# Optimization experiments

Hardware: AMD Instinct MI355X
Metric: run time of the kernel (lower is better)

## Reference

```python
import jax, jax.numpy as jnp
import numpy as np

H = 256       # hidden_dim
DICT = 30     # dict_size
SOS = 1       # symb2int['<sos>']

def gru_cell(x, h, Wih, Whh, bih, bhh):
    # PyTorch GRU cell math
    gi = x @ Wih.T + bih
    gh = h @ Whh.T + bhh
    ir, iz, inn = jnp.split(gi, 3, axis=-1)
    hr, hz, hn = jnp.split(gh, 3, axis=-1)
    r = jax.nn.sigmoid(ir + hr)
    z = jax.nn.sigmoid(iz + hz)
    n = jnp.tanh(inn + r * hn)
    return (1.0 - z) * n + z * h

def run_gru(xs, h0, Wih, Whh, bih, bhh):
    # xs: [T, B, F] -> outputs [T, B, Hc], final hidden [B, Hc]
    def step(h, x):
        h = gru_cell(x, h, Wih, Whh, bih, bhh)
        return h, h
    hT, out = jax.lax.scan(step, h0, xs)
    return out, hT

def setup_inputs() -> dict:
    key = jax.random.key(0)
    ks = jax.random.split(key, 24)
    B, T, L = 128, 512, 64
    se = 1.0 / np.sqrt(H)        # encoder GRU init scale
    sd = 1.0 / np.sqrt(2 * H)    # decoder GRU / linears scale
    def r(k, shape, sc):
        return jax.random.normal(k, shape, jnp.float32) * sc
    return {
        "x": jax.random.normal(ks[0], (B, T, 2), jnp.float32),
        "target_seq": jax.random.randint(ks[1], (B, L), 0, DICT),
        # encoder GRU, forward direction
        "enc_Wih_f": r(ks[2], (3 * H, 2), se), "enc_Whh_f": r(ks[3], (3 * H, H), se),
        "enc_bih_f": r(ks[4], (3 * H,), se),   "enc_bhh_f": r(ks[5], (3 * H,), se),
        # encoder GRU, backward direction
        "enc_Wih_b": r(ks[6], (3 * H, 2), se), "enc_Whh_b": r(ks[7], (3 * H, H), se),
        "enc_bih_b": r(ks[8], (3 * H,), se),   "enc_bhh_b": r(ks[9], (3 * H,), se),
        # decoder embedding + GRU (hidden 2H)
        "emb": r(ks[10], (DICT, H), 1.0),
        "dec_Wih": r(ks[11], (6 * H, H), sd),     "dec_Whh": r(ks[12], (6 * H, 2 * H), sd),
        "dec_bih": r(ks[13], (6 * H,), sd),       "dec_bhh": r(ks[14], (6 * H,), sd),
        # hidden2query, att_combine, fc
        "Wq": r(ks[15], (2 * H, 2 * H), sd), "bq": r(ks[16], (2 * H,), sd),
        "Wc": r(ks[17], (H, 4 * H), sd),     "bc": r(ks[18], (H,), sd),
        "Wf": r(ks[19], (DICT, H), se),      "bf": r(ks[20], (DICT,), se),
    }

def reference(x, target_seq,
              enc_Wih_f, enc_Whh_f, enc_bih_f, enc_bhh_f,
              enc_Wih_b, enc_Whh_b, enc_bih_b, enc_bhh_b,
              emb, dec_Wih, dec_Whh, dec_bih, dec_bhh,
              Wq, bq, Wc, bc, Wf, bf):
    B = x.shape[0]
    xs = jnp.transpose(x, (1, 0, 2))                # [T, B, 2]
    h0 = jnp.zeros((B, H), x.dtype)
    out_f, hf = run_gru(xs, h0, enc_Wih_f, enc_Whh_f, enc_bih_f, enc_bhh_f)
    out_b, hb = run_gru(xs[::-1], h0, enc_Wih_b, enc_Whh_b, enc_bih_b, enc_bhh_b)
    enc_out = jnp.concatenate([out_f, out_b[::-1]], axis=-1)  # [T, B, 2H]
    enc_out = jnp.transpose(enc_out, (1, 0, 2))               # [B, T, 2H]
    hidden = jnp.concatenate([hf, hb], axis=-1)               # [B, 2H]

    # teacher-forced decoder inputs: <sos>, target[0], ..., target[L-2]
    sos = jnp.full((B, 1), SOS, target_seq.dtype)
    toks = jnp.concatenate([sos, target_seq[:, :-1]], axis=1).T  # [L, B]

    def dec_step(h, tok):
        e = emb[tok]                                           # [B, H]
        h = gru_cell(e, h, dec_Wih, dec_Whh, dec_bih, dec_bhh) # [B, 2H]
        q = h @ Wq.T + bq                                      # hidden2query
        w = jax.nn.softmax(jnp.einsum('bh,bth->bt', q, enc_out), axis=-1)
        ctx = jnp.einsum('bt,bth->bh', w, enc_out)             # [B, 2H]
        o = jnp.concatenate([h, ctx], axis=-1) @ Wc.T + bc     # att_combine
        logits = o @ Wf.T + bf                                 # fc
        return h, (logits, w)

    hT, (logits, ws) = jax.lax.scan(dec_step, hidden, toks)
    vec_out = jnp.transpose(logits, (1, 0, 2))   # [B, L, DICT]
    attn = jnp.transpose(ws, (1, 2, 0))          # [B, T, L]
    return vec_out, hT[None], attn
```

## Files before the change

kernel.cpp:

```cpp
#include <hip/hip_runtime.h>
#include <hip/hip_bf16.h>

typedef unsigned int u32;
typedef unsigned short u16;
typedef _Float16 f16;
typedef f16 f16x2 __attribute__((ext_vector_type(2)));

#define BB 128
#define TT 512
#define HE 256
#define G3E 768
#define HD 512
#define G3D 1536
#define LL 64
#define NDICT 30
#define EMBD 256

__device__ __forceinline__ float fexp2(float v){
#if __has_builtin(__builtin_amdgcn_exp2f)
  return __builtin_amdgcn_exp2f(v);
#else
  return exp2f(v);
#endif
}
__device__ __forceinline__ float frcp(float v){
#if __has_builtin(__builtin_amdgcn_rcpf)
  return __builtin_amdgcn_rcpf(v);
#else
  return 1.f/v;
#endif
}
__device__ __forceinline__ float sigm(float v){
  return frcp(1.f + fexp2(-1.4426950408889634f*v));
}
__device__ __forceinline__ float ftanh(float v){
  float e = fexp2(fminf(v, 40.f)*2.8853901631790583f);
  return (e - 1.f)*frcp(e + 1.f);
}
__device__ __forceinline__ u16 f2h(float f){ return __builtin_bit_cast(u16, (f16)f); }
__device__ __forceinline__ float h2f(u16 b){ return (float)__builtin_bit_cast(f16, b); }
__device__ __forceinline__ u32 pkh2(float a, float b){
  u16 lo = __builtin_bit_cast(u16, (f16)a);
  u16 hi = __builtin_bit_cast(u16, (f16)b);
  return (u32)lo | ((u32)hi << 16);
}
__device__ __forceinline__ u32 pkrtz(float a, float b){
  return __builtin_bit_cast(u32, __builtin_amdgcn_cvt_pkrtz(a, b));
}
__device__ __forceinline__ f16x2 bc2(u32 v){ return __builtin_bit_cast(f16x2, v); }

__device__ __forceinline__ void unp8h(uint4 v, float* d){
  f16x2 p;
  p = bc2(v.x); d[0]=(float)p.x; d[1]=(float)p.y;
  p = bc2(v.y); d[2]=(float)p.x; d[3]=(float)p.y;
  p = bc2(v.z); d[4]=(float)p.x; d[5]=(float)p.y;
  p = bc2(v.w); d[6]=(float)p.x; d[7]=(float)p.y;
}
__device__ __forceinline__ ushort4 hpk4(float a, float b, float c, float d){
  ushort4 r; r.x=f2h(a); r.y=f2h(b); r.z=f2h(c); r.w=f2h(d); return r;
}

__device__ __forceinline__ float dot2f(u32 w, f16x2 h, float acc){
#if __has_builtin(__builtin_amdgcn_fdot2)
  return __builtin_amdgcn_fdot2(__builtin_bit_cast(f16x2, w), h, acc, false);
#else
  f16x2 wv = __builtin_bit_cast(f16x2, w);
  acc = fmaf((float)wv.x, (float)h.x, acc);
  return fmaf((float)wv.y, (float)h.y, acc);
#endif
}
__device__ __forceinline__ float dot2h(u32 a, u32 b, float acc){
  return dot2f(a, bc2(b), acc);
}
__device__ __forceinline__ void dot_u4(uint4 wv, uint4 hv, float& acc){
  acc = dot2f(wv.x, bc2(hv.x), acc);
  acc = dot2f(wv.y, bc2(hv.y), acc);
  acc = dot2f(wv.z, bc2(hv.z), acc);
  acc = dot2f(wv.w, bc2(hv.w), acc);
}

#define INNER16(Q0,Q1)                                              \
  _Pragma("unroll 8")                                               \
  for (int k = 0; k < 32; ++k){                                     \
    float4 a4 = *(const float4*)&A_s[k*68 + (Q0)*4];                \
    float4 b4 = *(const float4*)&B_s[k*68 + (Q1)*4];                \
    acc[0] =fmaf(a4.x,b4.x,acc[0]);  acc[1] =fmaf(a4.x,b4.y,acc[1]); \
    acc[2] =fmaf(a4.x,b4.z,acc[2]);  acc[3] =fmaf(a4.x,b4.w,acc[3]); \
    acc[4] =fmaf(a4.y,b4.x,acc[4]);  acc[5] =fmaf(a4.y,b4.y,acc[5]); \
    acc[6] =fmaf(a4.y,b4.z,acc[6]);  acc[7] =fmaf(a4.y,b4.w,acc[7]); \
    acc[8] =fmaf(a4.z,b4.x,acc[8]);  acc[9] =fmaf(a4.z,b4.y,acc[9]); \
    acc[10]=fmaf(a4.z,b4.z,acc[10]); acc[11]=fmaf(a4.z,b4.w,acc[11]);\
    acc[12]=fmaf(a4.w,b4.x,acc[12]); acc[13]=fmaf(a4.w,b4.y,acc[13]);\
    acc[14]=fmaf(a4.w,b4.z,acc[14]); acc[15]=fmaf(a4.w,b4.w,acc[15]);\
  }

#define INNER8P(Q0,Q1)                                                  \
  _Pragma("unroll")                                                     \
  for (int kp = 0; kp < 16; ++kp){                                      \
    uint4 a2 = *(const uint4*)&A2_s[kp*68 + (Q0)*4];                    \
    uint4 b2 = *(const uint4*)&B2_s[kp*68 + (Q1)*4];                    \
    acc[0] =dot2h(a2.x,b2.x,acc[0]);  acc[1] =dot2h(a2.x,b2.y,acc[1]);  \
    acc[2] =dot2h(a2.x,b2.z,acc[2]);  acc[3] =dot2h(a2.x,b2.w,acc[3]);  \
    acc[4] =dot2h(a2.y,b2.x,acc[4]);  acc[5] =dot2h(a2.y,b2.y,acc[5]);  \
    acc[6] =dot2h(a2.y,b2.z,acc[6]);  acc[7] =dot2h(a2.y,b2.w,acc[7]);  \
    acc[8] =dot2h(a2.z,b2.x,acc[8]);  acc[9] =dot2h(a2.z,b2.y,acc[9]);  \
    acc[10]=dot2h(a2.z,b2.z,acc[10]); acc[11]=dot2h(a2.z,b2.w,acc[11]); \
    acc[12]=dot2h(a2.w,b2.x,acc[12]); acc[13]=dot2h(a2.w,b2.y,acc[13]); \
    acc[14]=dot2h(a2.w,b2.z,acc[14]); acc[15]=dot2h(a2.w,b2.w,acc[15]); \
  }

__global__ __launch_bounds__(256) void k_prep_pairT(const float* __restrict__ src,
                                                    u32* __restrict__ dst, int N, int K){
  int idx = blockIdx.x*256 + threadIdx.x;
  int KP = K >> 1;
  if (idx < N*KP){
    int n = idx / KP, kp = idx - n*KP;
    dst[(size_t)kp*N + n] = pkh2(src[(size_t)n*K + 2*kp], src[(size_t)n*K + 2*kp + 1]);
  }
}

__global__ __launch_bounds__(256) void k_prep_wenc(const float* __restrict__ WF,
                                                   const float* __restrict__ WB,
                                                   uint4* __restrict__ dst){
  int idx = blockIdx.x*256 + threadIdx.x;
  int dir = idx / 24576, rem = idx - dir*24576;
  int i = rem / 768, j = rem - i*768;
  const float* s = (dir ? WB : WF) + (size_t)j*HE + i*8;
  uint4 v; v.x=pkh2(s[0],s[1]); v.y=pkh2(s[2],s[3]); v.z=pkh2(s[4],s[5]); v.w=pkh2(s[6],s[7]);
  dst[idx] = v;
}

__global__ __launch_bounds__(256) void k_prep_wdec(const float* __restrict__ src,
                                                   uint4* __restrict__ dst){
  int idx = blockIdx.x*256 + threadIdx.x;
  int lane = idx & 63;
  int ci = lane & 7, kq = lane >> 3;
  int rest = idx >> 6;
  int u = rest & 7, g = (rest >> 3) % 3, cg = rest / 24;
  int row = g*512 + cg*8 + ci;
  int col = kq*64 + u*8;
  const float* s = src + (size_t)row*HD + col;
  uint4 v; v.x=pkh2(s[0],s[1]); v.y=pkh2(s[2],s[3]); v.z=pkh2(s[4],s[5]); v.w=pkh2(s[6],s[7]);
  dst[idx] = v;
}

__global__ __launch_bounds__(256) void k_gi_tab(const float* __restrict__ emb,
                                                const float* __restrict__ Wih,
                                                const float* __restrict__ bih,
                                                float* __restrict__ gi){
  int v = blockIdx.x, gy = blockIdx.y;
  int g = gy*256 + threadIdx.x;
  __shared__ float e_s[EMBD];
  if (threadIdx.x < EMBD) e_s[threadIdx.x] = emb[(size_t)v*EMBD + threadIdx.x];
  __syncthreads();
  const float4* w4 = (const float4*)(Wih + (size_t)g*EMBD);
  float acc = 0.f;
  #pragma unroll 8
  for (int k = 0; k < EMBD/4; ++k){
    float4 w = w4[k];
    float4 h = *(const float4*)&e_s[k*4];
    acc = fmaf(w.x,h.x,fmaf(w.y,h.y,fmaf(w.z,h.z,fmaf(w.w,h.w,acc))));
  }
  gi[(size_t)v*G3D + g] = acc + bih[g];
}

__global__ __launch_bounds__(256) void k_h0cvt(const float* __restrict__ src,
                                               f16* __restrict__ dst){
  int i = blockIdx.x*256 + threadIdx.x;
  dst[i] = (f16)src[i];
}

__global__ __launch_bounds__(768, 3) void k_enc_p(
    const float* __restrict__ x,
    const uint4* __restrict__ Wp,
    const float* __restrict__ WihF, const float* __restrict__ WihB,
    const float* __restrict__ bihF, const float* __restrict__ bhhF,
    const float* __restrict__ bihB, const float* __restrict__ bhhB,
    u16* __restrict__ enc_out, float* __restrict__ h0out)
{
  const int b   = blockIdx.x >> 1;
  const int dir = blockIdx.x & 1;
  const int j   = threadIdx.x;
  const float* Wih = dir ? WihB : WihF;
  const float* bih = dir ? bihB : bihF;
  const float* bhh = dir ? bhhB : bhhF;

  __shared__ __align__(16) f16 h_lds[HE];
  __shared__ float gh[2*HE];
  __shared__ float gin_s[HE], ghn_s[HE];

  uint4 w[32];
  {
    const uint4* wsrc = Wp + (size_t)dir*24576 + j;
    #pragma unroll
    for (int i = 0; i < 32; ++i) w[i] = wsrc[(size_t)i*768];
  }
  const float wv0r = Wih[j*2+0], wv1r = Wih[j*2+1];
  const float bi = bih[j], bh = bhh[j];
  const float badd = bi + bh;
  if (j < HE) h_lds[j] = (f16)0.f;
  float h_own = 0.f;
  __syncthreads();

  for (int t = 0; t < TT; ++t){
    const int tt = dir ? (TT-1-t) : t;
    const float x0 = x[((size_t)b*TT + tt)*2 + 0];
    const float x1 = x[((size_t)b*TT + tt)*2 + 1];

    float a0=0.f, a1=0.f, a2=0.f, a3=0.f;
    const uint4* hv = (const uint4*)h_lds;
    #pragma unroll
    for (int i = 0; i < 32; ++i){
      uint4 h4 = hv[i];
      uint4 wi = w[i];
      a0 = dot2f(wi.x, bc2(h4.x), a0);
      a1 = dot2f(wi.y, bc2(h4.y), a1);
      a2 = dot2f(wi.z, bc2(h4.z), a2);
      a3 = dot2f(wi.w, bc2(h4.w), a3);
    }
    const float acc = (a0+a1)+(a2+a3);
    const float xp = fmaf(wv0r, x0, wv1r*x1);
    if (j < 2*HE){
      gh[j] = acc + xp + badd;
    } else {
      ghn_s[j-2*HE] = acc + bh;
      gin_s[j-2*HE] = xp + bi;
    }
    __syncthreads();
    if (j < HE){
      float r = sigm(gh[j]);
      float z = sigm(gh[j+HE]);
      float n = ftanh(gin_s[j] + r*ghn_s[j]);
      float hnew = (1.f - z)*n + z*h_own;
      h_own = hnew;
      h_lds[j] = (f16)hnew;
      enc_out[((size_t)b*TT + tt)*HD + dir*HE + j] = f2h(hnew);
    }
    __syncthreads();
  }
  if (j < HE) h0out[(size_t)b*HD + dir*HE + j] = h_own;
}

__global__ __launch_bounds__(256, 2) void k_dstep(
    const int* __restrict__ tgt, const float* __restrict__ gi_tab,
    const uint4* __restrict__ Wd2, const float* __restrict__ bhh,
    const f16* __restrict__ h_prev, f16* __restrict__ h_next,
    float* __restrict__ Hall, int l)
{
  const int bg = blockIdx.x & 3, cg = blockIdx.x >> 2;
  const int tid = threadIdx.x;
  const int ci = tid & 7, kq = (tid >> 3) & 7, bq = tid >> 6;

  __shared__ __align__(16) f16 h_s[32][HD];
  __shared__ float p_s[3][32][8][8];
  __shared__ int tok_s[32];

  uint4 w[24];
  {
    const uint4* wp = Wd2 + (size_t)cg*24*64 + (kq*8 + ci);
    #pragma unroll
    for (int i = 0; i < 24; ++i) w[i] = wp[(size_t)i*64];
  }
  {
    const uint4* hsrc = (const uint4*)(h_prev + (size_t)bg*32*HD);
    uint4* hdst = (uint4*)&h_s[0][0];
    #pragma unroll
    for (int i = 0; i < 8; ++i) hdst[tid + i*256] = hsrc[tid + i*256];
  }
  if (tid < 32) tok_s[tid] = (l == 0) ? 1 : tgt[(size_t)(bg*32 + tid)*LL + l - 1];
  __syncthreads();

  #pragma unroll
  for (int nb = 0; nb < 8; ++nb){
    const int b = bq*8 + nb;
    const uint4* hv = (const uint4*)&h_s[b][kq*64];
    float x0 = 0.f, x1 = 0.f, x2 = 0.f;
    #pragma unroll
    for (int u = 0; u < 8; ++u){
      uint4 hh = hv[u];
      dot_u4(w[u],      hh, x0);
      dot_u4(w[8 + u],  hh, x1);
      dot_u4(w[16 + u], hh, x2);
    }
    p_s[0][b][ci][kq] = x0;
    p_s[1][b][ci][kq] = x1;
    p_s[2][b][ci][kq] = x2;
  }
  __syncthreads();

  {
    const int b = tid >> 3, cl = tid & 7;
    const int C = cg*8 + cl;
    float s0 = 0.f, s1 = 0.f, s2 = 0.f;
    #pragma unroll
    for (int k = 0; k < 8; ++k){
      s0 += p_s[0][b][cl][k];
      s1 += p_s[1][b][cl][k];
      s2 += p_s[2][b][cl][k];
    }
    const int tok = tok_s[b];
    const float* gp = gi_tab + (size_t)tok*G3D + C;
    float r = sigm(gp[0]    + s0 + bhh[C]);
    float z = sigm(gp[HD]   + s1 + bhh[HD + C]);
    float n = ftanh(gp[2*HD] + r*(s2 + bhh[2*HD + C]));
    float hp = (float)h_s[b][C];
    float hnew = (1.f - z)*n + z*hp;
    const int gb = bg*32 + b;
    h_next[(size_t)gb*HD + C] = (f16)hnew;
    Hall[((size_t)l*BB + gb)*HD + C] = hnew;
  }
}

__global__ __launch_bounds__(256) void k_query(const float* __restrict__ Hall,
                                               const u32* __restrict__ Wq2,
                                               const float* __restrict__ bq,
                                               u16* __restrict__ Qh){
  const int rt = blockIdx.x, nt = blockIdx.y;
  const int tid = threadIdx.x;
  __shared__ u32 A2_s[16*68];
  __shared__ u32 B2_s[16*68];
  const int rq = tid >> 4, nq = tid & 15;
  const int i = tid >> 2, jj = tid & 3;
  const int i3 = tid >> 4, n4 = tid & 15;
  float acc[16] = {};
  for (int kc = 0; kc < 16; ++kc){
    __syncthreads();
    {
      const float* src = Hall + (size_t)(rt*64 + i)*HD + kc*32 + jj*8;
      float4 v0 = *(const float4*)src, v1 = *(const float4*)(src+4);
      A2_s[(jj*4+0)*68+i] = pkrtz(v0.x, v0.y);
      A2_s[(jj*4+1)*68+i] = pkrtz(v0.z, v0.w);
      A2_s[(jj*4+2)*68+i] = pkrtz(v1.x, v1.y);
      A2_s[(jj*4+3)*68+i] = pkrtz(v1.z, v1.w);
    }
    {
      uint4 v = *(const uint4*)(Wq2 + (size_t)(kc*16 + i3)*HD + nt*64 + n4*4);
      *(uint4*)&B2_s[i3*68 + n4*4] = v;
    }
    __syncthreads();
    INNER8P(rq, nq)
  }
  const int n0 = nt*64 + nq*4;
  float4 bv = *(const float4*)&bq[n0];
  #pragma unroll
  for (int r = 0; r < 4; ++r){
    u16* dst = Qh + (size_t)(rt*64 + rq*4 + r)*HD + n0;
    *(ushort4*)dst = hpk4(acc[r*4+0]+bv.x, acc[r*4+1]+bv.y,
                          acc[r*4+2]+bv.z, acc[r*4+3]+bv.w);
  }
}

__global__ __launch_bounds__(256) void k_scores(const u16* __restrict__ Qh,
                                                const u16* __restrict__ enc,
                                                float* __restrict__ Sbuf){
  const int bI = blockIdx.x, tt = blockIdx.y;
  const int tid = threadIdx.x;
  __shared__ u32 A2_s[16*68];
  __shared__ u32 B2_s[16*68];
  const int lq = tid >> 4, tq = tid & 15;
  const int i = tid >> 2, jj = tid & 3;
  float acc[16] = {};
  for (int kc = 0; kc < 16; ++kc){
    __syncthreads();
    {
      uint4 va = *(const uint4*)(Qh + ((size_t)i*BB + bI)*HD + kc*32 + jj*8);
      A2_s[(jj*4+0)*68+i] = va.x;
      A2_s[(jj*4+1)*68+i] = va.y;
      A2_s[(jj*4+2)*68+i] = va.z;
      A2_s[(jj*4+3)*68+i] = va.w;
    }
    {
      uint4 vb = *(const uint4*)(enc + ((size_t)bI*TT + tt*64 + i)*HD + kc*32 + jj*8);
      B2_s[(jj*4+0)*68+i] = vb.x;
      B2_s[(jj*4+1)*68+i] = vb.y;
      B2_s[(jj*4+2)*68+i] = vb.z;
      B2_s[(jj*4+3)*68+i] = vb.w;
    }
    __syncthreads();
    INNER8P(lq, tq)
  }
  #pragma unroll
  for (int r = 0; r < 4; ++r){
    float4 o = make_float4(acc[r*4+0],acc[r*4+1],acc[r*4+2],acc[r*4+3]);
    *(float4*)&Sbuf[((size_t)bI*LL + lq*4+r)*TT + tt*64 + tq*4] = o;
  }
}

__global__ __launch_bounds__(64) void k_softmax(const float* __restrict__ Sbuf,
                                                u16* __restrict__ Ph){
  const int row = blockIdx.x;
  const int lane = threadIdx.x;
  const float* s = Sbuf + (size_t)row*TT;
  float v[8]; float m = -1e30f;
  #pragma unroll
  for (int i = 0; i < 8; ++i){ v[i] = s[lane + i*64]; m = fmaxf(m, v[i]); }
  #pragma unroll
  for (int o = 32; o; o >>= 1) m = fmaxf(m, __shfl_xor(m, o));
  float Z = 0.f;
  #pragma unroll
  for (int i = 0; i < 8; ++i){ v[i] = fexp2(1.4426950408889634f*(v[i] - m)); Z += v[i]; }
  #pragma unroll
  for (int o = 32; o; o >>= 1) Z += __shfl_xor(Z, o);
  float inv = frcp(Z);
  u16* p = Ph + (size_t)row*TT;
  #pragma unroll
  for (int i = 0; i < 8; ++i) p[lane + i*64] = f2h(v[i]*inv);
}

__global__ __launch_bounds__(256) void k_attn_tr(const u16* __restrict__ Ph,
                                                 float* __restrict__ att){
  const int bI = blockIdx.x, tt = blockIdx.y;
  const int tid = threadIdx.x;
  __shared__ u16 tile[64][72];
  {
    const int i = tid >> 2, jj = tid & 3;
    #pragma unroll
    for (int rep = 0; rep < 2; ++rep){
      int ch = jj + rep*4;
      uint4 v = *(const uint4*)(Ph + ((size_t)bI*LL + i)*TT + tt*64 + ch*8);
      *(uint4*)&tile[i][ch*8] = v;
    }
  }
  __syncthreads();
  const int t = tid >> 2, jl = tid & 3;
  #pragma unroll
  for (int rep = 0; rep < 4; ++rep){
    int l0 = jl*16 + rep*4;
    float4 o;
    o.x = h2f(tile[l0+0][t]); o.y = h2f(tile[l0+1][t]);
    o.z = h2f(tile[l0+2][t]); o.w = h2f(tile[l0+3][t]);
    *(float4*)&att[((size_t)bI*TT + tt*64 + t)*LL + l0] = o;
  }
}

__global__ __launch_bounds__(256) void k_ctx(const u16* __restrict__ Ph,
                                             const u16* __restrict__ enc,
                                             u16* __restrict__ ctxh){
  const int bI = blockIdx.x, nt = blockIdx.y;
  const int tid = threadIdx.x;
  __shared__ float A_s[32*68];
  __shared__ float B_s[32*68];
  const int lq = tid >> 4, nq = tid & 15;
  const int i = tid >> 2, jj = tid & 3;
  const int i2 = tid >> 3, jj2 = tid & 7;
  float acc[16] = {};
  for (int tc = 0; tc < 16; ++tc){
    __syncthreads();
    {
      float tmp[8];
      uint4 va = *(const uint4*)(Ph + ((size_t)bI*LL + i)*TT + tc*32 + jj*8);
      unp8h(va, tmp);
      #pragma unroll
      for (int m = 0; m < 8; ++m) A_s[(jj*8+m)*68 + i] = tmp[m];
    }
    {
      float tmp[8];
      uint4 vb = *(const uint4*)(enc + ((size_t)bI*TT + tc*32 + i2)*HD + nt*64 + jj2*8);
      unp8h(vb, tmp);
      *(float4*)&B_s[i2*68 + jj2*8]     = make_float4(tmp[0],tmp[1],tmp[2],tmp[3]);
      *(float4*)&B_s[i2*68 + jj2*8 + 4] = make_float4(tmp[4],tmp[5],tmp[6],tmp[7]);
    }
    __syncthreads();
    INNER16(lq, nq)
  }
  const int n0 = nt*64 + nq*4;
  #pragma unroll
  for (int r = 0; r < 4; ++r){
    int ll = lq*4 + r;
    u16* dst = ctxh + ((size_t)ll*BB + bI)*HD + n0;
    *(ushort4*)dst = hpk4(acc[r*4+0], acc[r*4+1], acc[r*4+2], acc[r*4+3]);
  }
}

__global__ __launch_bounds__(256) void k_outc(const float* __restrict__ Hall,
                                              const u16* __restrict__ ctxh,
                                              const u32* __restrict__ Wc2,
                                              const float* __restrict__ bc,
                                              float* __restrict__ obuf){
  const int rt = blockIdx.x, nt = blockIdx.y;
  const int tid = threadIdx.x;
  __shared__ u32 A2_s[16*68];
  __shared__ u32 B2_s[16*68];
  const int rq = tid >> 4, nq = tid & 15;
  const int i = tid >> 2, jj = tid & 3;
  const int i3 = tid >> 4, n4 = tid & 15;
  float acc[16] = {};
  for (int kc = 0; kc < 32; ++kc){
    __syncthreads();
    if (kc < 16){
      const float* src = Hall + (size_t)(rt*64 + i)*HD + kc*32 + jj*8;
      float4 v0 = *(const float4*)src, v1 = *(const float4*)(src+4);
      A2_s[(jj*4+0)*68+i] = pkrtz(v0.x, v0.y);
      A2_s[(jj*4+1)*68+i] = pkrtz(v0.z, v0.w);
      A2_s[(jj*4+2)*68+i] = pkrtz(v1.x, v1.y);
      A2_s[(jj*4+3)*68+i] = pkrtz(v1.z, v1.w);
    } else {
      uint4 v = *(const uint4*)(ctxh + (size_t)(rt*64 + i)*HD + (kc-16)*32 + jj*8);
      A2_s[(jj*4+0)*68+i] = v.x;
      A2_s[(jj*4+1)*68+i] = v.y;
      A2_s[(jj*4+2)*68+i] = v.z;
      A2_s[(jj*4+3)*68+i] = v.w;
    }
    {
      uint4 v = *(const uint4*)(Wc2 + (size_t)(kc*16 + i3)*256 + nt*64 + n4*4);
      *(uint4*)&B2_s[i3*68 + n4*4] = v;
    }
    __syncthreads();
    INNER8P(rq, nq)
  }
  const int n0 = nt*64 + nq*4;
  float4 bv = *(const float4*)&bc[n0];
  #pragma unroll
  for (int r = 0; r < 4; ++r){
    float4 o = make_float4(acc[r*4+0]+bv.x, acc[r*4+1]+bv.y,
                           acc[r*4+2]+bv.z, acc[r*4+3]+bv.w);
    *(float4*)&obuf[(size_t)(rt*64 + rq*4 + r)*256 + n0] = o;
  }
}

__global__ __launch_bounds__(256) void k_fc(const float* __restrict__ obuf,
                                            const float* __restrict__ Wf,
                                            const float* __restrict__ bfv,
                                            float* __restrict__ out_vec){
  const int rt = blockIdx.x;
  const int tid = threadIdx.x;
  __shared__ float w_s[30*260];
  for (int rr = 0; rr < 30; ++rr) w_s[rr*260 + tid] = Wf[(size_t)rr*256 + tid];
  __syncthreads();
  const int rl = tid >> 2, dq = tid & 3;
  const int r = rt*64 + rl;
  float acc[8] = {};
  for (int k = 0; k < 256; k += 4){
    float4 o4 = *(const float4*)&obuf[(size_t)r*256 + k];
    #pragma unroll
    for (int jq = 0; jq < 8; ++jq){
      int d = dq*8 + jq;
      if (d < 30){
        float4 w4 = *(const float4*)&w_s[d*260 + k];
        acc[jq] = fmaf(o4.x,w4.x,fmaf(o4.y,w4.y,fmaf(o4.z,w4.z,fmaf(o4.w,w4.w,acc[jq]))));
      }
    }
  }
  const int b = r & 127, l = r >> 7;
  #pragma unroll
  for (int jq = 0; jq < 8; ++jq){
    int d = dq*8 + jq;
    if (d < 30) out_vec[((size_t)b*LL + l)*NDICT + d] = acc[jq] + bfv[d];
  }
}

__global__ __launch_bounds__(256) void k_copy(const float* __restrict__ src,
                                              float* __restrict__ dst, int n){
  int i = blockIdx.x*256 + threadIdx.x;
  if (i < n) dst[i] = src[i];
}

extern "C" void kernel_launch(void* const* d_in, const int* in_sizes, int n_in,
                              void* d_out, int out_size, void* d_ws, size_t ws_size,
                              hipStream_t stream)
{
  const float* x     = (const float*)d_in[0];
  const int*   tgt   = (const int*)  d_in[1];
  const float* eWihF = (const float*)d_in[2];
  const float* eWhhF = (const float*)d_in[3];
  const float* ebihF = (const float*)d_in[4];
  const float* ebhhF = (const float*)d_in[5];
  const float* eWihB = (const float*)d_in[6];
  const float* eWhhB = (const float*)d_in[7];
  const float* ebihB = (const float*)d_in[8];
  const float* ebhhB = (const float*)d_in[9];
  const float* emb   = (const float*)d_in[10];
  const float* dWih  = (const float*)d_in[11];
  const float* dWhh  = (const float*)d_in[12];
  const float* dbih  = (const float*)d_in[13];
  const float* dbhh  = (const float*)d_in[14];
  const float* Wq    = (const float*)d_in[15];
  const float* bq    = (const float*)d_in[16];
  const float* Wc    = (const float*)d_in[17];
  const float* bc    = (const float*)d_in[18];
  const float* Wf    = (const float*)d_in[19];
  const float* bfv   = (const float*)d_in[20];

  char* w = (char*)d_ws;
  uint4* Wpenc = (uint4*)w; w += 786432;
  uint4* Wpdec = (uint4*)w; w += 1572864;
  u32*   Wq2   = (u32*)w;  w += 524288;
  u32*   Wc2   = (u32*)w;  w += 524288;
  float* gi_t  = (float*)w; w += 184320;
  float* h0buf = (float*)w; w += 262144;
  f16*   h16A  = (f16*)w; w += 131072;
  f16*   h16B  = (f16*)w; w += 131072;
  float* Hall  = (float*)w; w += 16777216;
  u16*   Qh    = (u16*)w;
  u16*   Ph    = (u16*)w; w += 8388608;
  float* Sbuf  = (float*)w;
  u16*   ctxh  = (u16*)w; w += 8388608;
  float* obuf  = (float*)w; w += 8388608;
  u16*   ench  = (u16*)w; w += 67108864;

  float* out     = (float*)d_out;
  float* out_vec = out;
  float* out_hT  = out + (size_t)BB*LL*NDICT;
  float* out_att = out_hT + (size_t)BB*HD;

  k_prep_wenc<<<192, 256, 0, stream>>>(eWhhF, eWhhB, Wpenc);
  k_prep_wdec<<<384, 256, 0, stream>>>(dWhh, Wpdec);
  k_prep_pairT<<<512, 256, 0, stream>>>(Wq, Wq2, HD, HD);
  k_prep_pairT<<<512, 256, 0, stream>>>(Wc, Wc2, 256, 1024);
  k_gi_tab<<<dim3(NDICT, 6), 256, 0, stream>>>(emb, dWih, dbih, gi_t);

  k_enc_p<<<BB*2, G3E, 0, stream>>>(x, Wpenc, eWihF, eWihB,
                                    ebihF, ebhhF, ebihB, ebhhB, ench, h0buf);

  k_h0cvt<<<256, 256, 0, stream>>>(h0buf, h16A);
  for (int l = 0; l < LL; ++l){
    const f16* hp = (l & 1) ? h16B : h16A;
    f16*       hn = (l & 1) ? h16A : h16B;
    k_dstep<<<256, 256, 0, stream>>>(tgt, gi_t, Wpdec, dbhh, hp, hn, Hall, l);
  }

  k_query<<<dim3(128,8), 256, 0, stream>>>(Hall, Wq2, bq, Qh);
  k_scores<<<dim3(128,8), 256, 0, stream>>>(Qh, ench, Sbuf);
  k_softmax<<<BB*LL, 64, 0, stream>>>(Sbuf, Ph);
  k_attn_tr<<<dim3(128,8), 256, 0, stream>>>(Ph, out_att);
  k_ctx<<<dim3(128,8), 256, 0, stream>>>(Ph, ench, ctxh);
  k_outc<<<dim3(128,4), 256, 0, stream>>>(Hall, ctxh, Wc2, bc, obuf);
  k_fc<<<BB, 256, 0, stream>>>(obuf, Wf, bfv, out_vec);
  k_copy<<<(BB*HD+255)/256, 256, 0, stream>>>(Hall + (size_t)63*BB*HD, out_hT, BB*HD);
}
```

Measured before the change: 1.222 ms.

## Split encoder recurrent matvec across 8-lane groups with shuffle reduction

The encoder GRU step no longer has each thread read the whole 256-wide hidden vector from LDS. Each lane in a group of 8 now reads only its own 32-element slice of a padded hidden buffer and computes partial dots for 8 rows. The partials are combined with a butterfly of xor shuffles so each thread ends with its own row's total. This cuts LDS read traffic per step and uses padding to avoid bank conflicts, at the cost of extra shuffles and a reshuffled weight layout in the prep kernel.

```diff
diff --git a/kernel.cpp b/kernel.cpp
--- a/kernel.cpp
+++ b/kernel.cpp
@@ -124,8 +124,10 @@
                                                    uint4* __restrict__ dst){
   int idx = blockIdx.x*256 + threadIdx.x;
   int dir = idx / 24576, rem = idx - dir*24576;
-  int i = rem / 768, j = rem - i*768;
-  const float* s = (dir ? WB : WF) + (size_t)j*HE + i*8;
+  int i = rem / 768, t = rem - i*768;
+  int rg = t >> 3, cg = t & 7;
+  int r = i >> 2, q = i & 3;
+  const float* s = (dir ? WB : WF) + (size_t)(rg*8 + r)*HE + cg*32 + q*8;
   uint4 v; v.x=pkh2(s[0],s[1]); v.y=pkh2(s[2],s[3]); v.z=pkh2(s[4],s[5]); v.w=pkh2(s[6],s[7]);
   dst[idx] = v;
 }
@@ -181,11 +183,12 @@
   const int b   = blockIdx.x >> 1;
   const int dir = blockIdx.x & 1;
   const int j   = threadIdx.x;
+  const int cg  = j & 7;
   const float* Wih = dir ? WihB : WihF;
   const float* bih = dir ? bihB : bihF;
   const float* bhh = dir ? bhhB : bhhF;
 
-  __shared__ __align__(16) f16 h_lds[HE];
+  __shared__ __align__(16) f16 h_pad[8*40];
   __shared__ float gh[2*HE];
   __shared__ float gin_s[HE], ghn_s[HE];
 
@@ -198,8 +201,9 @@
   const float wv0r = Wih[j*2+0], wv1r = Wih[j*2+1];
   const float bi = bih[j], bh = bhh[j];
   const float badd = bi + bh;
-  if (j < HE) h_lds[j] = (f16)0.f;
+  if (j < HE) h_pad[(j >> 5)*40 + (j & 31)] = (f16)0.f;
   float h_own = 0.f;
+  const bool s0 = (cg & 1), s1 = (cg & 2), s2 = (cg & 4);
   __syncthreads();
 
   for (int t = 0; t < TT; ++t){
@@ -207,23 +211,31 @@
     const float x0 = x[((size_t)b*TT + tt)*2 + 0];
     const float x1 = x[((size_t)b*TT + tt)*2 + 1];
 
-    float a0=0.f, a1=0.f, a2=0.f, a3=0.f;
-    const uint4* hv = (const uint4*)h_lds;
-    #pragma unroll
-    for (int i = 0; i < 32; ++i){
-      uint4 h4 = hv[i];
-      uint4 wi = w[i];
-      a0 = dot2f(wi.x, bc2(h4.x), a0);
-      a1 = dot2f(wi.y, bc2(h4.y), a1);
-      a2 = dot2f(wi.z, bc2(h4.z), a2);
-      a3 = dot2f(wi.w, bc2(h4.w), a3);
-    }
-    const float acc = (a0+a1)+(a2+a3);
+    const uint4* hv = (const uint4*)(h_pad + cg*40);
+    uint4 h0 = hv[0], h1 = hv[1], h2 = hv[2], h3 = hv[3];
+    float p[8];
+    #pragma unroll
+    for (int r = 0; r < 8; ++r){
+      float a = 0.f;
+      dot_u4(w[r*4+0], h0, a);
+      dot_u4(w[r*4+1], h1, a);
+      dot_u4(w[r*4+2], h2, a);
+      dot_u4(w[r*4+3], h3, a);
+      p[r] = a;
+    }
+    float q0 = (s0 ? p[1] : p[0]) + __shfl_xor(s0 ? p[0] : p[1], 1);
+    float q1 = (s0 ? p[3] : p[2]) + __shfl_xor(s0 ? p[2] : p[3], 1);
+    float q2 = (s0 ? p[5] : p[4]) + __shfl_xor(s0 ? p[4] : p[5], 1);
+    float q3 = (s0 ? p[7] : p[6]) + __shfl_xor(s0 ? p[6] : p[7], 1);
+    float r0 = (s1 ? q1 : q0) + __shfl_xor(s1 ? q0 : q1, 2);
+    float r1 = (s1 ? q3 : q2) + __shfl_xor(s1 ? q2 : q3, 2);
+    float tot = (s2 ? r1 : r0) + __shfl_xor(s2 ? r0 : r1, 4);
+
     const float xp = fmaf(wv0r, x0, wv1r*x1);
     if (j < 2*HE){
-      gh[j] = acc + xp + badd;
+      gh[j] = tot + xp + badd;
     } else {
-      ghn_s[j-2*HE] = acc + bh;
+      ghn_s[j-2*HE] = tot + bh;
       gin_s[j-2*HE] = xp + bi;
     }
     __syncthreads();
@@ -233,7 +245,7 @@
       float n = ftanh(gin_s[j] + r*ghn_s[j]);
       float hnew = (1.f - z)*n + z*h_own;
       h_own = hnew;
-      h_lds[j] = (f16)hnew;
+      h_pad[(j >> 5)*40 + (j & 31)] = (f16)hnew;
       enc_out[((size_t)b*TT + tt)*HD + dir*HE + j] = f2h(hnew);
     }
     __syncthreads();
```

New measurement: 1.213 ms. No clear change (-0.8%).
